# Optimization experiments

Measured on AMD Instinct MI355X. Metric: run time of the kernel, lower is better.

The kernel has to match this reference:

```python
import jax, jax.numpy as jnp
import numpy as np

EPS = 1e-6
H = 16  # num_heads

def _ln(x):
    mu = jnp.mean(x, axis=-1, keepdims=True)
    var = jnp.mean(jnp.square(x - mu), axis=-1, keepdims=True)
    return (x - mu) / jnp.sqrt(var + EPS)

def _mod(x, shift, scale):  # shift/scale: [B,D]
    return x * (1.0 + scale[:, None, :]) + shift[:, None, :]

def _heads(x, qkv_w, qkv_b):
    B, N, C = x.shape
    hd = C // H
    qkv = (x @ qkv_w + qkv_b).reshape(B, N, 3, H, hd).transpose(2, 0, 3, 1, 4)
    return qkv[0], qkv[1], qkv[2]  # each [B,H,N,hd]

def _attend(q, k, v):
    sc = (q.shape[-1]) ** -0.5
    a = jax.nn.softmax(jnp.einsum('bhnd,bhmd->bhnm', q, k) * sc, axis=-1)
    o = jnp.einsum('bhnm,bhmd->bhnd', a, v)
    B, h, N, hd = o.shape
    return o.transpose(0, 2, 1, 3).reshape(B, N, h * hd)

def _mha(x, qkv_w, qkv_b, proj_w, proj_b):
    q, k, v = _heads(x, qkv_w, qkv_b)
    return _attend(q, k, v) @ proj_w + proj_b

def setup_inputs() -> dict:
    key = jax.random.key(0)
    ks = jax.random.split(key, 16)
    B, T, D = 2, 2048, 1024
    Dh = 4 * D
    s = 0.02
    return {
        'x': jax.random.normal(ks[0], (B, T, D), jnp.float32),
        'c': jax.random.normal(ks[1], (B, 2, D), jnp.float32),
        'attn_qkv_w': jax.random.normal(ks[2], (D, 3 * D), jnp.float32) * s,
        'attn_qkv_b': jnp.zeros((3 * D,), jnp.float32),
        'attn_proj_w': jax.random.normal(ks[3], (D, D), jnp.float32) * s,
        'attn_proj_b': jnp.zeros((D,), jnp.float32),
        'crs_qkv_w': jax.random.normal(ks[4], (D, 3 * D), jnp.float32) * s,
        'crs_qkv_b': jnp.zeros((3 * D,), jnp.float32),
        'crs_proj_w': jax.random.normal(ks[5], (D, D), jnp.float32) * s,
        'crs_proj_b': jnp.zeros((D,), jnp.float32),
        'mlp_fc1_w': jax.random.normal(ks[6], (D, Dh), jnp.float32) * s,
        'mlp_fc1_b': jnp.zeros((Dh,), jnp.float32),
        'mlp_fc2_w': jax.random.normal(ks[7], (Dh, D), jnp.float32) * s,
        'mlp_fc2_b': jnp.zeros((D,), jnp.float32),
        'ada_w': jax.random.normal(ks[8], (D, 9 * D), jnp.float32) * s,
        'ada_b': jnp.zeros((9 * D,), jnp.float32),
    }

def reference(x, c, attn_qkv_w, attn_qkv_b, attn_proj_w, attn_proj_b,
              crs_qkv_w, crs_qkv_b, crs_proj_w, crs_proj_b,
              mlp_fc1_w, mlp_fc1_b, mlp_fc2_w, mlp_fc2_b, ada_w, ada_b):
    # adaLN-zero modulation: SiLU + Linear -> 9 chunks of [B,2,D]
    mod = jax.nn.silu(c) @ ada_w + ada_b
    (sh_msa, sc_msa, g_msa, sh_mca, sc_mca, g_mca,
     sh_mlp, sc_mlp, g_mlp) = jnp.split(mod, 9, axis=2)
    B, T, D = x.shape
    h = T // 2
    x0, x1 = x[:, :h], x[:, h:]
    # self-attention on each half with its own shift/scale/gate
    x0 = x0 + g_msa[:, 0][:, None, :] * _mha(_mod(_ln(x0), sh_msa[:, 0], sc_msa[:, 0]),
                                             attn_qkv_w, attn_qkv_b, attn_proj_w, attn_proj_b)
    x1 = x1 + g_msa[:, 1][:, None, :] * _mha(_mod(_ln(x1), sh_msa[:, 1], sc_msa[:, 1]),
                                             attn_qkv_w, attn_qkv_b, attn_proj_w, attn_proj_b)
    # two-way cross-attention
    xm = _mod(_ln(x0), sh_mca[:, 0], sc_mca[:, 0])
    ym = _mod(_ln(x1), sh_mca[:, 1], sc_mca[:, 1])
    qx, kx, vx = _heads(xm, crs_qkv_w, crs_qkv_b)
    qy, ky, vy = _heads(ym, crs_qkv_w, crs_qkv_b)
    ox = _attend(qx, ky, vy) @ crs_proj_w + crs_proj_b
    oy = _attend(qy, kx, vx) @ crs_proj_w + crs_proj_b
    x = x + jnp.concatenate((g_mca[:, 0][:, None, :] * ox,
                             g_mca[:, 1][:, None, :] * oy), axis=1)
    # gated MLP on each half
    def mlp(z):
        return jax.nn.gelu(z @ mlp_fc1_w + mlp_fc1_b, approximate=True) @ mlp_fc2_w + mlp_fc2_b
    m0 = mlp(_mod(_ln(x[:, :h]), sh_mlp[:, 0], sc_mlp[:, 0]))
    m1 = mlp(_mod(_ln(x[:, h:]), sh_mlp[:, 1], sc_mlp[:, 1]))
    x = x + jnp.concatenate((g_mlp[:, 0][:, None, :] * m0,
                             g_mlp[:, 1][:, None, :] * m1), axis=1)
    return x
```

## Files before the change

### kernel.cpp

```cpp
#include <hip/hip_runtime.h>
#include <hip/hip_bf16.h>

#define BB 2
#define TT 2048
#define DD 1024
#define NH 16
#define HALF 1024
#define DHID 4096
#define ND9 9216
#define ROWS (BB*TT)

using bf16 = __hip_bfloat16;
typedef short bf16x8 __attribute__((ext_vector_type(8)));
typedef float f32x4 __attribute__((ext_vector_type(4)));
typedef unsigned short u16;

__device__ __forceinline__ float b2f(bf16 v){ return __bfloat162float(v); }
__device__ __forceinline__ bf16 f2b(float v){ return __float2bfloat16(v); }
__device__ __forceinline__ float bits2f(u16 b){ return __uint_as_float(((unsigned)b) << 16); }
__device__ __forceinline__ u16 fb(float v){
    unsigned u = __float_as_uint(v);
    u += 0x7fffu + ((u >> 16) & 1u);
    return (u16)(u >> 16);
}
__device__ __forceinline__ void gl_lds16(const u16* g, u16* l) {
    __builtin_amdgcn_global_load_lds(
        (const __attribute__((address_space(1))) unsigned int*)g,
        (__attribute__((address_space(3))) unsigned int*)l, 16, 0, 0);
}

__global__ void ada_part(const float* __restrict__ c, const float* __restrict__ ada_w,
                         float* __restrict__ part) {
    __shared__ float sc_[4][64];
    int s = blockIdx.y;
    int k0 = s * 64;
    int n0 = blockIdx.x * 1024 + threadIdx.x * 4;
    {
        int r = threadIdx.x >> 6, k = threadIdx.x & 63;
        float v = c[r*DD + k0 + k];
        sc_[r][k] = v / (1.f + __expf(-v));
    }
    __syncthreads();
    float4 a0 = {0,0,0,0}, a1 = {0,0,0,0}, a2 = {0,0,0,0}, a3 = {0,0,0,0};
    for (int k = 0; k < 64; ++k) {
        float4 wv = *(const float4*)&ada_w[(size_t)(k0 + k)*ND9 + n0];
        float s0 = sc_[0][k], s1 = sc_[1][k], s2 = sc_[2][k], s3 = sc_[3][k];
        a0.x += s0*wv.x; a0.y += s0*wv.y; a0.z += s0*wv.z; a0.w += s0*wv.w;
        a1.x += s1*wv.x; a1.y += s1*wv.y; a1.z += s1*wv.z; a1.w += s1*wv.w;
        a2.x += s2*wv.x; a2.y += s2*wv.y; a2.z += s2*wv.z; a2.w += s2*wv.w;
        a3.x += s3*wv.x; a3.y += s3*wv.y; a3.z += s3*wv.z; a3.w += s3*wv.w;
    }
    *(float4*)&part[((size_t)(s*4 + 0))*ND9 + n0] = a0;
    *(float4*)&part[((size_t)(s*4 + 1))*ND9 + n0] = a1;
    *(float4*)&part[((size_t)(s*4 + 2))*ND9 + n0] = a2;
    *(float4*)&part[((size_t)(s*4 + 3))*ND9 + n0] = a3;
}

__global__ void ada_reduce(const float* __restrict__ part, const float* __restrict__ ada_b,
                           float* __restrict__ mod) {
    int g = blockIdx.x * 1024 + threadIdx.x * 4;
    int r = g / ND9, n = g - r*ND9;
    float4 acc = *(const float4*)&ada_b[n];
    #pragma unroll
    for (int s = 0; s < 16; ++s) {
        float4 p = *(const float4*)&part[((size_t)(s*4 + r))*ND9 + n];
        acc.x += p.x; acc.y += p.y; acc.z += p.z; acc.w += p.w;
    }
    *(float4*)&mod[(size_t)r*ND9 + n] = acc;
}

__global__ void cast_x4(const float* __restrict__ x, float* __restrict__ xc) {
    int i = (blockIdx.x * 256 + threadIdx.x) * 4;
    *(float4*)&xc[i] = *(const float4*)&x[i];
}

__global__ void resid_add(const float* __restrict__ src, const u16* __restrict__ gv,
                          float* __restrict__ dst) {
    int i = (blockIdx.x * 256 + threadIdx.x) * 4;
    float4 s = *(const float4*)&src[i];
    ushort4 g = *(const ushort4*)&gv[i];
    float4 o;
    o.x = s.x + bits2f(g.x); o.y = s.y + bits2f(g.y);
    o.z = s.z + bits2f(g.z); o.w = s.w + bits2f(g.w);
    *(float4*)&dst[i] = o;
}

__global__ void transpose_w(const float* __restrict__ W, u16* __restrict__ Wt, int K, int N) {
    __shared__ float T[32][33];
    int n0 = blockIdx.x * 32, k0 = blockIdx.y * 32;
    int lx = threadIdx.x & 31, ly = threadIdx.x >> 5;
    #pragma unroll
    for (int i = 0; i < 4; ++i)
        T[ly + i*8][lx] = W[(size_t)(k0 + ly + i*8)*N + n0 + lx];
    __syncthreads();
    #pragma unroll
    for (int i = 0; i < 4; ++i) {
        int n = ly + i*8;
        Wt[(size_t)(n0 + n)*K + k0 + lx] = fb(T[lx][n]);
    }
}

__global__ void vtrans(const u16* __restrict__ qkv, u16* __restrict__ vt) {
    __shared__ u16 T[64][72];
    int kt = blockIdx.x;
    int gh = blockIdx.y;
    int tid = threadIdx.x;
    int key = tid >> 2, c8 = (tid & 3) * 16;
    const u16* src = qkv + (size_t)((gh >> 4)*1024 + kt*64 + key)*3072 + 2048 + (gh & 15)*64 + c8;
    *(uint4*)&T[key][c8]     = *(const uint4*)src;
    *(uint4*)&T[key][c8 + 8] = *(const uint4*)(src + 8);
    __syncthreads();
    int d = tid >> 2, kc = (tid & 3) * 16;
    u16 tmp[16];
    #pragma unroll
    for (int i = 0; i < 16; ++i) tmp[i] = T[kc + i][d];
    u16* dst = vt + ((size_t)gh*64 + d)*1024 + kt*64 + kc;
    *(uint4*)&dst[0] = *(const uint4*)&tmp[0];
    *(uint4*)&dst[8] = *(const uint4*)&tmp[8];
}

__global__ void ln_mod_kernel(const float* __restrict__ xc, const float* __restrict__ mod,
                              int jshift, int jscale, bf16* __restrict__ y) {
    int row = blockIdx.x;
    int b = row / TT, t = row % TT;
    int cz = (t >= HALF) ? 1 : 0;
    const float* mp = mod + (size_t)(b*2 + cz) * ND9;
    const float* xr = xc + (size_t)row * DD;
    int tid = threadIdx.x;
    float v[4];
    float s = 0.f, ss = 0.f;
    #pragma unroll
    for (int i = 0; i < 4; ++i) {
        v[i] = xr[tid + i*256];
        s += v[i]; ss += v[i]*v[i];
    }
    __shared__ float red[256];
    red[tid] = s; __syncthreads();
    for (int o = 128; o > 0; o >>= 1) { if (tid < o) red[tid] += red[tid+o]; __syncthreads(); }
    float mean = red[0] * (1.f/DD);
    __syncthreads();
    red[tid] = ss; __syncthreads();
    for (int o = 128; o > 0; o >>= 1) { if (tid < o) red[tid] += red[tid+o]; __syncthreads(); }
    float var = red[0] * (1.f/DD) - mean*mean;
    float rstd = rsqrtf(var + 1e-6f);
    bf16* yr = y + (size_t)row * DD;
    #pragma unroll
    for (int i = 0; i < 4; ++i) {
        int d = tid + i*256;
        float sh = mp[jshift*DD + d], sc2 = mp[jscale*DD + d];
        yr[d] = f2b((v[i] - mean) * rstd * (1.f + sc2) + sh);
    }
}

__device__ __forceinline__ void epi_store(u16* out, int o_off, int N, int mm, int n, float v,
                                          const float* mod, int jg, int epi) {
    if (epi == 0) {
        out[(size_t)(mm - o_off)*N + n] = fb(v);
    } else if (epi == 1) {
        float u = v;
        float g = 0.5f*u*(1.f + tanhf(0.7978845608028654f*(u + 0.044715f*u*u*u)));
        out[(size_t)(mm - o_off)*N + n] = fb(g);
    } else {
        int brow = mm / TT, tt2 = mm % TT;
        int cz = (tt2 >= HALF) ? 1 : 0;
        const float* mp = mod + (size_t)(brow*2 + cz)*ND9 + (size_t)jg*DD;
        out[(size_t)(mm - o_off)*N + n] = fb(mp[n]*v);
    }
}

__global__ __launch_bounds__(256, 2) void gemm_mfma(
    const u16* __restrict__ A, const u16* __restrict__ Wt, const float* __restrict__ bias,
    u16* __restrict__ out, const float* __restrict__ mod, int jg,
    int m_base, int a_off, int o_off, int K, int N, int epi)
{
    __shared__ u16 As[128*32];
    __shared__ u16 Bs[128*32];
    int tid = threadIdx.x;
    int w = tid >> 6, lane = tid & 63;
    int quad = lane >> 4, l16 = lane & 15;
    int m0 = m_base + blockIdx.y * 128;
    int n0 = blockIdx.x * 128;
    int wr = (w & 1) * 64, wc = (w >> 1) * 64;

    f32x4 acc[4][4];
    #pragma unroll
    for (int i = 0; i < 4; ++i)
        #pragma unroll
        for (int j = 0; j < 4; ++j) acc[i][j] = (f32x4){0.f,0.f,0.f,0.f};

    const u16* Ag = A + (size_t)(m0 - a_off) * K;
    const u16* Bg = Wt + (size_t)n0 * K;
    int srow = lane >> 2, scol = (lane & 3) * 8;
    int c0 = w*2, c1 = w*2 + 1;

    for (int k0 = 0; k0 < K; k0 += 32) {
        gl_lds16(Ag + (size_t)(c0*16 + srow)*K + k0 + scol, As + c0*512);
        gl_lds16(Ag + (size_t)(c1*16 + srow)*K + k0 + scol, As + c1*512);
        gl_lds16(Bg + (size_t)(c0*16 + srow)*K + k0 + scol, Bs + c0*512);
        gl_lds16(Bg + (size_t)(c1*16 + srow)*K + k0 + scol, Bs + c1*512);
        __syncthreads();
        bf16x8 af[4], bfr[4];
        #pragma unroll
        for (int i = 0; i < 4; ++i) af[i] = *(const bf16x8*)&As[(wr + i*16 + l16)*32 + quad*8];
        #pragma unroll
        for (int j = 0; j < 4; ++j) bfr[j] = *(const bf16x8*)&Bs[(wc + j*16 + l16)*32 + quad*8];
        #pragma unroll
        for (int i = 0; i < 4; ++i)
            #pragma unroll
            for (int j = 0; j < 4; ++j)
                acc[i][j] = __builtin_amdgcn_mfma_f32_16x16x32_bf16(af[i], bfr[j], acc[i][j], 0, 0, 0);
        __syncthreads();
    }

    #pragma unroll
    for (int i = 0; i < 4; ++i)
        #pragma unroll
        for (int r = 0; r < 4; ++r) {
            int mm = m0 + wr + i*16 + quad*4 + r;
            #pragma unroll
            for (int j = 0; j < 4; ++j) {
                int n = n0 + wc + j*16 + l16;
                epi_store(out, o_off, N, mm, n, acc[i][j][r] + bias[n], mod, jg, epi);
            }
        }
}

__global__ __launch_bounds__(256, 2) void gemm64(
    const u16* __restrict__ A, const u16* __restrict__ Wt, const float* __restrict__ bias,
    u16* __restrict__ out, const float* __restrict__ mod, int jg,
    int m_base, int a_off, int o_off, int K, int N, int epi)
{
    __shared__ u16 As[64*32];
    __shared__ u16 Bs[128*32];
    int tid = threadIdx.x;
    int w = tid >> 6, lane = tid & 63;
    int quad = lane >> 4, l16 = lane & 15;
    int m0 = m_base + blockIdx.y * 64;
    int n0 = blockIdx.x * 128;

    f32x4 acc[4][2];
    #pragma unroll
    for (int i = 0; i < 4; ++i)
        #pragma unroll
        for (int j = 0; j < 2; ++j) acc[i][j] = (f32x4){0.f,0.f,0.f,0.f};

    const u16* Ag = A + (size_t)(m0 - a_off) * K;
    const u16* Bg = Wt + (size_t)n0 * K;
    int srow = lane >> 2, scol = (lane & 3) * 8;

    for (int k0 = 0; k0 < K; k0 += 32) {
        gl_lds16(Ag + (size_t)(w*16 + srow)*K + k0 + scol, As + w*512);
        gl_lds16(Bg + (size_t)((w*2)*16 + srow)*K + k0 + scol, Bs + (w*2)*512);
        gl_lds16(Bg + (size_t)((w*2+1)*16 + srow)*K + k0 + scol, Bs + (w*2+1)*512);
        __syncthreads();
        bf16x8 af[4], bfr[2];
        #pragma unroll
        for (int i = 0; i < 4; ++i) af[i] = *(const bf16x8*)&As[(i*16 + l16)*32 + quad*8];
        #pragma unroll
        for (int j = 0; j < 2; ++j) bfr[j] = *(const bf16x8*)&Bs[(w*32 + j*16 + l16)*32 + quad*8];
        #pragma unroll
        for (int i = 0; i < 4; ++i)
            #pragma unroll
            for (int j = 0; j < 2; ++j)
                acc[i][j] = __builtin_amdgcn_mfma_f32_16x16x32_bf16(af[i], bfr[j], acc[i][j], 0, 0, 0);
        __syncthreads();
    }

    #pragma unroll
    for (int i = 0; i < 4; ++i)
        #pragma unroll
        for (int r = 0; r < 4; ++r) {
            int mm = m0 + i*16 + quad*4 + r;
            #pragma unroll
            for (int j = 0; j < 2; ++j) {
                int n = n0 + w*32 + j*16 + l16;
                epi_store(out, o_off, N, mm, n, acc[i][j][r] + bias[n], mod, jg, epi);
            }
        }
}

__global__ __launch_bounds__(256) void attn_mfma(const u16* __restrict__ qkv,
                                                 const u16* __restrict__ vt,
                                                 u16* __restrict__ attn_out, int kv_swap) {
    __shared__ u16 Ks[64][72];
    __shared__ u16 Vs[64][72];
    __shared__ u16 Ps[4][16][72];
    int qt = blockIdx.x, head = blockIdx.y, bh = blockIdx.z;
    int kvbh = kv_swap ? (bh ^ 1) : bh;
    int tid = threadIdx.x;
    int w = tid >> 6, lane = tid & 63;
    int quad = lane >> 4, l16 = lane & 15;
    int qrow0 = bh*1024 + qt*64 + w*16;

    const u16* qp = qkv + (size_t)(qrow0 + l16)*3072 + head*64;
    bf16x8 qa0 = *(const bf16x8*)(qp + quad*8);
    bf16x8 qa1 = *(const bf16x8*)(qp + 32 + quad*8);

    f32x4 oacc[4];
    #pragma unroll
    for (int i = 0; i < 4; ++i) oacc[i] = (f32x4){0.f,0.f,0.f,0.f};
    float mst[4], lst[4];
    #pragma unroll
    for (int r = 0; r < 4; ++r) { mst[r] = -3e38f; lst[r] = 0.f; }

    int skey = tid >> 2, sc8 = (tid & 3) * 16;
    const u16* kbase = qkv + (size_t)(kvbh*1024 + skey)*3072 + 1024 + head*64 + sc8;
    const u16* vbase = vt + ((size_t)(kvbh*16 + head)*64 + skey)*1024 + sc8;

    for (int kt = 0; kt < 16; ++kt) {
        __syncthreads();
        const u16* kp = kbase + (size_t)kt*64*3072;
        *(uint4*)&Ks[skey][sc8]     = *(const uint4*)kp;
        *(uint4*)&Ks[skey][sc8 + 8] = *(const uint4*)(kp + 8);
        const u16* vp = vbase + kt*64;
        *(uint4*)&Vs[skey][sc8]     = *(const uint4*)vp;
        *(uint4*)&Vs[skey][sc8 + 8] = *(const uint4*)(vp + 8);
        __syncthreads();

        f32x4 sacc[4];
        #pragma unroll
        for (int nt = 0; nt < 4; ++nt) sacc[nt] = (f32x4){0.f,0.f,0.f,0.f};
        #pragma unroll
        for (int nt = 0; nt < 4; ++nt) {
            bf16x8 kb0 = *(const bf16x8*)&Ks[nt*16 + l16][quad*8];
            bf16x8 kb1 = *(const bf16x8*)&Ks[nt*16 + l16][32 + quad*8];
            sacc[nt] = __builtin_amdgcn_mfma_f32_16x16x32_bf16(qa0, kb0, sacc[nt], 0, 0, 0);
            sacc[nt] = __builtin_amdgcn_mfma_f32_16x16x32_bf16(qa1, kb1, sacc[nt], 0, 0, 0);
        }
        #pragma unroll
        for (int r = 0; r < 4; ++r) {
            float sv0 = sacc[0][r]*0.125f, sv1 = sacc[1][r]*0.125f;
            float sv2 = sacc[2][r]*0.125f, sv3 = sacc[3][r]*0.125f;
            float mx = fmaxf(fmaxf(sv0, sv1), fmaxf(sv2, sv3));
            #pragma unroll
            for (int o = 1; o < 16; o <<= 1) mx = fmaxf(mx, __shfl_xor(mx, o));
            float mnew = fmaxf(mst[r], mx);
            float alpha = __expf(mst[r] - mnew);
            float p0 = __expf(sv0 - mnew), p1 = __expf(sv1 - mnew);
            float p2 = __expf(sv2 - mnew), p3 = __expf(sv3 - mnew);
            float ls = p0 + p1 + p2 + p3;
            #pragma unroll
            for (int o = 1; o < 16; o <<= 1) ls += __shfl_xor(ls, o);
            lst[r] = lst[r]*alpha + ls;
            mst[r] = mnew;
            #pragma unroll
            for (int dt = 0; dt < 4; ++dt) oacc[dt][r] *= alpha;
            int qr = quad*4 + r;
            Ps[w][qr][ 0 + l16] = fb(p0);
            Ps[w][qr][16 + l16] = fb(p1);
            Ps[w][qr][32 + l16] = fb(p2);
            Ps[w][qr][48 + l16] = fb(p3);
        }
        bf16x8 pa0 = *(const bf16x8*)&Ps[w][l16][quad*8];
        bf16x8 pa1 = *(const bf16x8*)&Ps[w][l16][32 + quad*8];
        #pragma unroll
        for (int dt = 0; dt < 4; ++dt) {
            bf16x8 vb0 = *(const bf16x8*)&Vs[dt*16 + l16][quad*8];
            bf16x8 vb1 = *(const bf16x8*)&Vs[dt*16 + l16][32 + quad*8];
            oacc[dt] = __builtin_amdgcn_mfma_f32_16x16x32_bf16(pa0, vb0, oacc[dt], 0, 0, 0);
            oacc[dt] = __builtin_amdgcn_mfma_f32_16x16x32_bf16(pa1, vb1, oacc[dt], 0, 0, 0);
        }
    }
    #pragma unroll
    for (int dt = 0; dt < 4; ++dt)
        #pragma unroll
        for (int r = 0; r < 4; ++r)
            attn_out[(size_t)(qrow0 + quad*4 + r)*DD + head*64 + dt*16 + l16] = fb(oacc[dt][r] / lst[r]);
}

extern "C" void kernel_launch(void* const* d_in, const int* in_sizes, int n_in,
                              void* d_out, int out_size, void* d_ws, size_t ws_size,
                              hipStream_t stream) {
    const float* x          = (const float*)d_in[0];
    const float* c          = (const float*)d_in[1];
    const float* attn_qkv_w = (const float*)d_in[2];
    const float* attn_qkv_b = (const float*)d_in[3];
    const float* attn_proj_w= (const float*)d_in[4];
    const float* attn_proj_b= (const float*)d_in[5];
    const float* crs_qkv_w  = (const float*)d_in[6];
    const float* crs_qkv_b  = (const float*)d_in[7];
    const float* crs_proj_w = (const float*)d_in[8];
    const float* crs_proj_b = (const float*)d_in[9];
    const float* fc1_w      = (const float*)d_in[10];
    const float* fc1_b      = (const float*)d_in[11];
    const float* fc2_w      = (const float*)d_in[12];
    const float* fc2_b      = (const float*)d_in[13];
    const float* ada_w      = (const float*)d_in[14];
    const float* ada_b      = (const float*)d_in[15];
    float* out = (float*)d_out;

    char* ws = (char*)d_ws;
    float* mod = (float*)ws;
    char* R1   = ws + (256u<<10);
    char* Yr   = R1 + (16u<<20);
    char* AOr  = Yr + (8u<<20);
    char* BIGr = AOr + (8u<<20);

    float* x0x1  = (float*)R1;
    u16*   wt_a  = (u16*)R1;
    u16*   vt    = (u16*)(R1 + (8u<<20));
    bf16*  y     = (bf16*)Yr;
    u16*   wt_p  = (u16*)Yr;
    u16*   attn_o= (u16*)AOr;
    u16*   big   = (u16*)BIGr;
    u16*   gvB   = (u16*)BIGr;
    u16*   gvY   = (u16*)Yr;
    u16*   hstage= (u16*)AOr;
    u16*   fc1_t = (u16*)R1;
    u16*   fc2_t = (u16*)(R1 + (8u<<20));
    float* apart = (float*)BIGr;

    ada_part<<<dim3(9, 16), 256, 0, stream>>>(c, ada_w, apart);
    ada_reduce<<<36, 256, 0, stream>>>(apart, ada_b, mod);
    cast_x4<<<4096, 256, 0, stream>>>(x, out);

    transpose_w<<<dim3(3*DD/32, DD/32), 256, 0, stream>>>(attn_qkv_w, wt_a, DD, 3*DD);
    ln_mod_kernel<<<ROWS, 256, 0, stream>>>(out, mod, 0, 1, y);
    gemm_mfma<<<dim3(3*DD/128, ROWS/128), 256, 0, stream>>>((const u16*)y, wt_a, attn_qkv_b,
                                                            big, nullptr, 0, 0, 0, 0, DD, 3*DD, 0);
    vtrans<<<dim3(16, 64), 256, 0, stream>>>(big, vt);
    attn_mfma<<<dim3(16, NH, 4), 256, 0, stream>>>(big, vt, attn_o, 0);
    transpose_w<<<dim3(DD/32, DD/32), 256, 0, stream>>>(attn_proj_w, wt_p, DD, DD);
    gemm64<<<dim3(DD/128, ROWS/64), 256, 0, stream>>>(attn_o, wt_p, attn_proj_b,
                                                      gvB, mod, 2, 0, 0, 0, DD, DD, 3);
    resid_add<<<4096, 256, 0, stream>>>(out, gvB, x0x1);

    ln_mod_kernel<<<ROWS, 256, 0, stream>>>(x0x1, mod, 3, 4, y);
    transpose_w<<<dim3(3*DD/32, DD/32), 256, 0, stream>>>(crs_qkv_w, wt_a, DD, 3*DD);
    gemm_mfma<<<dim3(3*DD/128, ROWS/128), 256, 0, stream>>>((const u16*)y, wt_a, crs_qkv_b,
                                                            big, nullptr, 0, 0, 0, 0, DD, 3*DD, 0);
    vtrans<<<dim3(16, 64), 256, 0, stream>>>(big, vt);
    attn_mfma<<<dim3(16, NH, 4), 256, 0, stream>>>(big, vt, attn_o, 1);
    transpose_w<<<dim3(DD/32, DD/32), 256, 0, stream>>>(crs_proj_w, wt_p, DD, DD);
    gemm64<<<dim3(DD/128, ROWS/64), 256, 0, stream>>>(attn_o, wt_p, crs_proj_b,
                                                      gvB, mod, 5, 0, 0, 0, DD, DD, 3);
    resid_add<<<4096, 256, 0, stream>>>(out, gvB, out);

    ln_mod_kernel<<<ROWS, 256, 0, stream>>>(out, mod, 6, 7, y);
    transpose_w<<<dim3(DHID/32, DD/32), 256, 0, stream>>>(fc1_w, fc1_t, DD, DHID);
    transpose_w<<<dim3(DD/32, DHID/32), 256, 0, stream>>>(fc2_w, fc2_t, DHID, DD);
    gemm_mfma<<<dim3(DHID/128, ROWS/128), 256, 0, stream>>>((const u16*)y, fc1_t, fc1_b,
                                                            hstage, nullptr, 0, 0, 0, 0, DD, DHID, 1);
    gemm64<<<dim3(DD/128, ROWS/64), 256, 0, stream>>>(hstage, fc2_t, fc2_b,
                                                      gvY, mod, 8, 0, 0, 0, DHID, DD, 3);
    resid_add<<<4096, 256, 0, stream>>>(out, gvY, out);
}
```

Baseline: 627.8 us.

## Fuse residual add into LayerNorm, widen GEMM K-tile to 64 with swizzled LDS

```diff
diff --git a/kernel.cpp b/kernel.cpp
--- a/kernel.cpp
+++ b/kernel.cpp
@@ -83,6 +83,43 @@
     o.x = s.x + bits2f(g.x); o.y = s.y + bits2f(g.y);
     o.z = s.z + bits2f(g.z); o.w = s.w + bits2f(g.w);
     *(float4*)&dst[i] = o;
+}
+
+__global__ void resid_ln(const float* __restrict__ src, const u16* __restrict__ gv,
+                         const float* __restrict__ mod, int jshift, int jscale,
+                         float* __restrict__ dstf, bf16* __restrict__ y) {
+    int row = blockIdx.x;
+    int b = row / TT, t = row % TT;
+    int cz = (t >= HALF) ? 1 : 0;
+    const float* mp = mod + (size_t)(b*2 + cz) * ND9;
+    int tid = threadIdx.x;
+    int d0 = tid * 4;
+    float4 s = *(const float4*)&src[(size_t)row*DD + d0];
+    float v[4] = {s.x, s.y, s.z, s.w};
+    if (gv) {
+        ushort4 g = *(const ushort4*)&gv[(size_t)row*DD + d0];
+        v[0] += bits2f(g.x); v[1] += bits2f(g.y); v[2] += bits2f(g.z); v[3] += bits2f(g.w);
+    }
+    if (dstf) *(float4*)&dstf[(size_t)row*DD + d0] = (float4){v[0], v[1], v[2], v[3]};
+    float sum = v[0]+v[1]+v[2]+v[3];
+    float ssq = v[0]*v[0]+v[1]*v[1]+v[2]*v[2]+v[3]*v[3];
+    __shared__ float red[256];
+    red[tid] = sum; __syncthreads();
+    for (int o = 128; o > 0; o >>= 1) { if (tid < o) red[tid] += red[tid+o]; __syncthreads(); }
+    float mean = red[0] * (1.f/DD);
+    __syncthreads();
+    red[tid] = ssq; __syncthreads();
+    for (int o = 128; o > 0; o >>= 1) { if (tid < o) red[tid] += red[tid+o]; __syncthreads(); }
+    float var = red[0] * (1.f/DD) - mean*mean;
+    float rstd = rsqrtf(var + 1e-6f);
+    float4 sh = *(const float4*)&mp[jshift*DD + d0];
+    float4 sc = *(const float4*)&mp[jscale*DD + d0];
+    ushort4 o4;
+    o4.x = fb((v[0]-mean)*rstd*(1.f+sc.x) + sh.x);
+    o4.y = fb((v[1]-mean)*rstd*(1.f+sc.y) + sh.y);
+    o4.z = fb((v[2]-mean)*rstd*(1.f+sc.z) + sh.z);
+    o4.w = fb((v[3]-mean)*rstd*(1.f+sc.w) + sh.w);
+    *(ushort4*)((u16*)y + (size_t)row*DD + d0) = o4;
 }
 
 __global__ void transpose_w(const float* __restrict__ W, u16* __restrict__ Wt, int K, int N) {
@@ -119,47 +156,13 @@
     *(uint4*)&dst[8] = *(const uint4*)&tmp[8];
 }
 
-__global__ void ln_mod_kernel(const float* __restrict__ xc, const float* __restrict__ mod,
-                              int jshift, int jscale, bf16* __restrict__ y) {
-    int row = blockIdx.x;
-    int b = row / TT, t = row % TT;
-    int cz = (t >= HALF) ? 1 : 0;
-    const float* mp = mod + (size_t)(b*2 + cz) * ND9;
-    const float* xr = xc + (size_t)row * DD;
-    int tid = threadIdx.x;
-    float v[4];
-    float s = 0.f, ss = 0.f;
-    #pragma unroll
-    for (int i = 0; i < 4; ++i) {
-        v[i] = xr[tid + i*256];
-        s += v[i]; ss += v[i]*v[i];
-    }
-    __shared__ float red[256];
-    red[tid] = s; __syncthreads();
-    for (int o = 128; o > 0; o >>= 1) { if (tid < o) red[tid] += red[tid+o]; __syncthreads(); }
-    float mean = red[0] * (1.f/DD);
-    __syncthreads();
-    red[tid] = ss; __syncthreads();
-    for (int o = 128; o > 0; o >>= 1) { if (tid < o) red[tid] += red[tid+o]; __syncthreads(); }
-    float var = red[0] * (1.f/DD) - mean*mean;
-    float rstd = rsqrtf(var + 1e-6f);
-    bf16* yr = y + (size_t)row * DD;
-    #pragma unroll
-    for (int i = 0; i < 4; ++i) {
-        int d = tid + i*256;
-        float sh = mp[jshift*DD + d], sc2 = mp[jscale*DD + d];
-        yr[d] = f2b((v[i] - mean) * rstd * (1.f + sc2) + sh);
-    }
-}
-
 __device__ __forceinline__ void epi_store(u16* out, int o_off, int N, int mm, int n, float v,
                                           const float* mod, int jg, int epi) {
     if (epi == 0) {
         out[(size_t)(mm - o_off)*N + n] = fb(v);
     } else if (epi == 1) {
-        float u = v;
-        float g = 0.5f*u*(1.f + tanhf(0.7978845608028654f*(u + 0.044715f*u*u*u)));
-        out[(size_t)(mm - o_off)*N + n] = fb(g);
+        float z = 0.7978845608028654f*(v + 0.044715f*v*v*v);
+        out[(size_t)(mm - o_off)*N + n] = fb(v / (1.f + __expf(-2.f*z)));
     } else {
         int brow = mm / TT, tt2 = mm % TT;
         int cz = (tt2 >= HALF) ? 1 : 0;
@@ -173,8 +176,8 @@
     u16* __restrict__ out, const float* __restrict__ mod, int jg,
     int m_base, int a_off, int o_off, int K, int N, int epi)
 {
-    __shared__ u16 As[128*32];
-    __shared__ u16 Bs[128*32];
+    __shared__ u16 As[128*64];
+    __shared__ u16 Bs[128*64];
     int tid = threadIdx.x;
     int w = tid >> 6, lane = tid & 63;
     int quad = lane >> 4, l16 = lane & 15;
@@ -190,25 +193,32 @@
 
     const u16* Ag = A + (size_t)(m0 - a_off) * K;
     const u16* Bg = Wt + (size_t)n0 * K;
-    int srow = lane >> 2, scol = (lane & 3) * 8;
-    int c0 = w*2, c1 = w*2 + 1;
-
-    for (int k0 = 0; k0 < K; k0 += 32) {
-        gl_lds16(Ag + (size_t)(c0*16 + srow)*K + k0 + scol, As + c0*512);
-        gl_lds16(Ag + (size_t)(c1*16 + srow)*K + k0 + scol, As + c1*512);
-        gl_lds16(Bg + (size_t)(c0*16 + srow)*K + k0 + scol, Bs + c0*512);
-        gl_lds16(Bg + (size_t)(c1*16 + srow)*K + k0 + scol, Bs + c1*512);
-        __syncthreads();
-        bf16x8 af[4], bfr[4];
-        #pragma unroll
-        for (int i = 0; i < 4; ++i) af[i] = *(const bf16x8*)&As[(wr + i*16 + l16)*32 + quad*8];
-        #pragma unroll
-        for (int j = 0; j < 4; ++j) bfr[j] = *(const bf16x8*)&Bs[(wc + j*16 + l16)*32 + quad*8];
-        #pragma unroll
-        for (int i = 0; i < 4; ++i)
-            #pragma unroll
-            for (int j = 0; j < 4; ++j)
-                acc[i][j] = __builtin_amdgcn_mfma_f32_16x16x32_bf16(af[i], bfr[j], acc[i][j], 0, 0, 0);
+    int srow = lane >> 3;
+    int scol = (((lane & 7) ^ ((lane >> 3) & 7))) * 8;
+    int xsw = (l16 & 7);
+
+    for (int k0 = 0; k0 < K; k0 += 64) {
+        #pragma unroll
+        for (int c = 0; c < 4; ++c) {
+            int ch = w*4 + c;
+            gl_lds16(Ag + (size_t)(ch*8 + srow)*K + k0 + scol, As + ch*512);
+            gl_lds16(Bg + (size_t)(ch*8 + srow)*K + k0 + scol, Bs + ch*512);
+        }
+        __syncthreads();
+        #pragma unroll
+        for (int kk = 0; kk < 2; ++kk) {
+            int pc = ((kk*4 + quad) ^ xsw) * 8;
+            bf16x8 af[4], bfr[4];
+            #pragma unroll
+            for (int i = 0; i < 4; ++i) af[i] = *(const bf16x8*)&As[(wr + i*16 + l16)*64 + pc];
+            #pragma unroll
+            for (int j = 0; j < 4; ++j) bfr[j] = *(const bf16x8*)&Bs[(wc + j*16 + l16)*64 + pc];
+            #pragma unroll
+            for (int i = 0; i < 4; ++i)
+                #pragma unroll
+                for (int j = 0; j < 4; ++j)
+                    acc[i][j] = __builtin_amdgcn_mfma_f32_16x16x32_bf16(af[i], bfr[j], acc[i][j], 0, 0, 0);
+        }
         __syncthreads();
     }
 
@@ -230,8 +240,8 @@
     u16* __restrict__ out, const float* __restrict__ mod, int jg,
     int m_base, int a_off, int o_off, int K, int N, int epi)
 {
-    __shared__ u16 As[64*32];
-    __shared__ u16 Bs[128*32];
+    __shared__ u16 As[64*64];
+    __shared__ u16 Bs[128*64];
     int tid = threadIdx.x;
     int w = tid >> 6, lane = tid & 63;
     int quad = lane >> 4, l16 = lane & 15;
@@ -246,23 +256,36 @@
 
     const u16* Ag = A + (size_t)(m0 - a_off) * K;
     const u16* Bg = Wt + (size_t)n0 * K;
-    int srow = lane >> 2, scol = (lane & 3) * 8;
-
-    for (int k0 = 0; k0 < K; k0 += 32) {
-        gl_lds16(Ag + (size_t)(w*16 + srow)*K + k0 + scol, As + w*512);
-        gl_lds16(Bg + (size_t)((w*2)*16 + srow)*K + k0 + scol, Bs + (w*2)*512);
-        gl_lds16(Bg + (size_t)((w*2+1)*16 + srow)*K + k0 + scol, Bs + (w*2+1)*512);
-        __syncthreads();
-        bf16x8 af[4], bfr[2];
-        #pragma unroll
-        for (int i = 0; i < 4; ++i) af[i] = *(const bf16x8*)&As[(i*16 + l16)*32 + quad*8];
-        #pragma unroll
-        for (int j = 0; j < 2; ++j) bfr[j] = *(const bf16x8*)&Bs[(w*32 + j*16 + l16)*32 + quad*8];
-        #pragma unroll
-        for (int i = 0; i < 4; ++i)
-            #pragma unroll
-            for (int j = 0; j < 2; ++j)
-                acc[i][j] = __builtin_amdgcn_mfma_f32_16x16x32_bf16(af[i], bfr[j], acc[i][j], 0, 0, 0);
+    int srow = lane >> 3;
+    int scol = (((lane & 7) ^ ((lane >> 3) & 7))) * 8;
+    int xsw = (l16 & 7);
+
+    for (int k0 = 0; k0 < K; k0 += 64) {
+        #pragma unroll
+        for (int c = 0; c < 2; ++c) {
+            int ch = w*2 + c;
+            gl_lds16(Ag + (size_t)(ch*8 + srow)*K + k0 + scol, As + ch*512);
+        }
+        #pragma unroll
+        for (int c = 0; c < 4; ++c) {
+            int ch = w*4 + c;
+            gl_lds16(Bg + (size_t)(ch*8 + srow)*K + k0 + scol, Bs + ch*512);
+        }
+        __syncthreads();
+        #pragma unroll
+        for (int kk = 0; kk < 2; ++kk) {
+            int pc = ((kk*4 + quad) ^ xsw) * 8;
+            bf16x8 af[4], bfr[2];
+            #pragma unroll
+            for (int i = 0; i < 4; ++i) af[i] = *(const bf16x8*)&As[(i*16 + l16)*64 + pc];
+            #pragma unroll
+            for (int j = 0; j < 2; ++j) bfr[j] = *(const bf16x8*)&Bs[(w*32 + j*16 + l16)*64 + pc];
+            #pragma unroll
+            for (int i = 0; i < 4; ++i)
+                #pragma unroll
+                for (int j = 0; j < 2; ++j)
+                    acc[i][j] = __builtin_amdgcn_mfma_f32_16x16x32_bf16(af[i], bfr[j], acc[i][j], 0, 0, 0);
+        }
         __syncthreads();
     }
 
@@ -396,7 +419,6 @@
     char* AOr  = Yr + (8u<<20);
     char* BIGr = AOr + (8u<<20);
 
-    float* x0x1  = (float*)R1;
     u16*   wt_a  = (u16*)R1;
     u16*   vt    = (u16*)(R1 + (8u<<20));
     bf16*  y     = (bf16*)Yr;
@@ -415,7 +437,7 @@
     cast_x4<<<4096, 256, 0, stream>>>(x, out);
 
     transpose_w<<<dim3(3*DD/32, DD/32), 256, 0, stream>>>(attn_qkv_w, wt_a, DD, 3*DD);
-    ln_mod_kernel<<<ROWS, 256, 0, stream>>>(out, mod, 0, 1, y);
+    resid_ln<<<ROWS, 256, 0, stream>>>(out, nullptr, mod, 0, 1, nullptr, y);
     gemm_mfma<<<dim3(3*DD/128, ROWS/128), 256, 0, stream>>>((const u16*)y, wt_a, attn_qkv_b,
                                                             big, nullptr, 0, 0, 0, 0, DD, 3*DD, 0);
     vtrans<<<dim3(16, 64), 256, 0, stream>>>(big, vt);
@@ -423,9 +445,8 @@
     transpose_w<<<dim3(DD/32, DD/32), 256, 0, stream>>>(attn_proj_w, wt_p, DD, DD);
     gemm64<<<dim3(DD/128, ROWS/64), 256, 0, stream>>>(attn_o, wt_p, attn_proj_b,
                                                       gvB, mod, 2, 0, 0, 0, DD, DD, 3);
-    resid_add<<<4096, 256, 0, stream>>>(out, gvB, x0x1);
-
-    ln_mod_kernel<<<ROWS, 256, 0, stream>>>(x0x1, mod, 3, 4, y);
+    resid_ln<<<ROWS, 256, 0, stream>>>(out, gvB, mod, 3, 4, nullptr, y);
+
     transpose_w<<<dim3(3*DD/32, DD/32), 256, 0, stream>>>(crs_qkv_w, wt_a, DD, 3*DD);
     gemm_mfma<<<dim3(3*DD/128, ROWS/128), 256, 0, stream>>>((const u16*)y, wt_a, crs_qkv_b,
                                                             big, nullptr, 0, 0, 0, 0, DD, 3*DD, 0);
@@ -434,9 +455,8 @@
     transpose_w<<<dim3(DD/32, DD/32), 256, 0, stream>>>(crs_proj_w, wt_p, DD, DD);
     gemm64<<<dim3(DD/128, ROWS/64), 256, 0, stream>>>(attn_o, wt_p, crs_proj_b,
                                                       gvB, mod, 5, 0, 0, 0, DD, DD, 3);
-    resid_add<<<4096, 256, 0, stream>>>(out, gvB, out);
-
-    ln_mod_kernel<<<ROWS, 256, 0, stream>>>(out, mod, 6, 7, y);
+    resid_ln<<<ROWS, 256, 0, stream>>>(out, gvB, mod, 6, 7, out, y);
+
     transpose_w<<<dim3(DHID/32, DD/32), 256, 0, stream>>>(fc1_w, fc1_t, DD, DHID);
     transpose_w<<<dim3(DD/32, DHID/32), 256, 0, stream>>>(fc2_w, fc2_t, DHID, DD);
     gemm_mfma<<<dim3(DHID/128, ROWS/128), 256, 0, stream>>>((const u16*)y, fc1_t, fc1_b,
```

New measurement: 609.7 us. 1.03x faster.
